# Kernel tuning notes

Hardware: AMD Instinct MI355X
Metric: run time of the kernel (lower is better)

Reference implementation:

```python
import jax, jax.numpy as jnp
import numpy as np

N_USERS = 50000
N_ENTITIES = 100000
N_NODES = N_USERS + N_ENTITIES
N_EDGES = 3000000
EMB_DIM = 64
WEIGHT_SIZES = [64, 64, 32, 16]  # [emb_dim] + weight_size
BATCH = 8192
LEAKY_SLOPE = 0.2  # KGAT (TF reference) uses leaky_relu alpha=0.2
EPS = 1e-12


def setup_inputs() -> dict:
    key = jax.random.key(0)
    ks = jax.random.split(key, 24)
    inp = {}
    inp["users"] = jax.random.randint(ks[0], (BATCH,), 0, N_USERS, dtype=jnp.int32)
    inp["pos_items"] = jax.random.randint(ks[1], (BATCH,), 0, N_ENTITIES, dtype=jnp.int32)
    inp["neg_items"] = jax.random.randint(ks[2], (BATCH,), 0, N_ENTITIES, dtype=jnp.int32)
    inp["all_h"] = jax.random.randint(ks[3], (N_EDGES,), 0, N_NODES, dtype=jnp.int32)
    inp["all_t"] = jax.random.randint(ks[4], (N_EDGES,), 0, N_NODES, dtype=jnp.int32)
    inp["A_values"] = jax.random.uniform(ks[5], (N_EDGES,), dtype=jnp.float32)
    inp["user_embed"] = jax.random.normal(ks[6], (N_USERS, EMB_DIM), dtype=jnp.float32) * 0.1
    inp["entity_embed"] = jax.random.normal(ks[7], (N_ENTITIES, EMB_DIM), dtype=jnp.float32) * 0.1
    ki = 8
    for k in range(3):
        din, dout = WEIGHT_SIZES[k], WEIGHT_SIZES[k + 1]
        scale = float(np.sqrt(2.0 / (din + dout)))  # xavier-ish
        inp[f"W_gc_{k}"] = jax.random.normal(ks[ki], (din, dout), dtype=jnp.float32) * scale; ki += 1
        inp[f"b_gc_{k}"] = jax.random.normal(ks[ki], (1, dout), dtype=jnp.float32) * scale; ki += 1
        inp[f"W_bi_{k}"] = jax.random.normal(ks[ki], (din, dout), dtype=jnp.float32) * scale; ki += 1
        inp[f"b_bi_{k}"] = jax.random.normal(ks[ki], (1, dout), dtype=jnp.float32) * scale; ki += 1
    return inp


def _bi_interaction(ego, all_h, all_t, A_values, layers, n_nodes):
    # KGAT bi-interaction aggregator over edge-list sparse adjacency.
    outs = [ego]
    for (W_gc, b_gc, W_bi, b_bi) in layers:
        # sparse A @ ego : gather tails, weight by attention, scatter-add to heads
        msgs = A_values[:, None] * ego[all_t]                       # [E, d]
        side = jax.ops.segment_sum(msgs, all_h, num_segments=n_nodes)  # [N, d]
        sum_emb = jax.nn.leaky_relu((ego + side) @ W_gc + b_gc, negative_slope=LEAKY_SLOPE)
        bi_emb = jax.nn.leaky_relu((ego * side) @ W_bi + b_bi, negative_slope=LEAKY_SLOPE)
        ego = sum_emb + bi_emb
        norm = ego / jnp.maximum(jnp.linalg.norm(ego, axis=1, keepdims=True), EPS)
        outs.append(norm)
    return jnp.concatenate(outs, axis=1)  # [N, 64+64+32+16]


def reference(users, pos_items, neg_items, all_h, all_t, A_values,
              user_embed, entity_embed,
              W_gc_0, b_gc_0, W_bi_0, b_bi_0,
              W_gc_1, b_gc_1, W_bi_1, b_bi_1,
              W_gc_2, b_gc_2, W_bi_2, b_bi_2):
    n_users = user_embed.shape[0]
    n_nodes = n_users + entity_embed.shape[0]
    ego = jnp.concatenate([user_embed, entity_embed], axis=0)  # [N, 64]
    layers = [(W_gc_0, b_gc_0, W_bi_0, b_bi_0),
              (W_gc_1, b_gc_1, W_bi_1, b_bi_1),
              (W_gc_2, b_gc_2, W_bi_2, b_bi_2)]
    all_emb = _bi_interaction(ego, all_h, all_t, A_values, layers, n_nodes)
    ua, ea = all_emb[:n_users], all_emb[n_users:]
    u_e = ua[users]
    pos_i_e = ea[pos_items]
    neg_i_e = ea[neg_items]
    return (u_e, pos_i_e, neg_i_e)
```

## Files before the change

kernel.cpp:

```cpp
#include <hip/hip_runtime.h>
#include <math.h>

#define N_USERS    50000
#define N_ENTITIES 100000
#define N_NODES    150000
#define N_EDGES    3000000
#define BATCH      8192
#define SLOPE      0.2f
#define EPSF       1e-12f

#define NBUK   2344
#define CAP    1536
#define STR    2560
#define PADM   16
#define BLK_E  12288
#define NPB    ((N_EDGES + BLK_E - 1) / BLK_E)
#define PBLK   1024
#define EPT    (BLK_E / PBLK)
#define CH     4096
#define PFW    (NBUK + 1)
#define CASTB  ((N_NODES * 64 / 4 + PBLK - 1) / PBLK)

__device__ __forceinline__ unsigned f2bf(float f) {
    unsigned u = __float_as_uint(f);
    return (u + 0x7FFFu + ((u >> 16) & 1u)) >> 16;
}
__device__ __forceinline__ float bf_lo(unsigned d) { return __uint_as_float(d << 16); }
__device__ __forceinline__ float bf_hi(unsigned d) { return __uint_as_float(d); }

__global__ __launch_bounds__(PBLK)
void prep_k(const int* __restrict__ all_h, const int* __restrict__ all_t,
            const float* __restrict__ A,
            int* __restrict__ prefix, int2* __restrict__ rec_src,
            const float* __restrict__ user_emb, const float* __restrict__ ent_emb,
            unsigned short* __restrict__ ego0_bf) {
    __shared__ int pos[NBUK];
    __shared__ int wsum[PBLK / 64];
    __shared__ int2 srec[CH];

    int t = threadIdx.x;

    if (blockIdx.x >= NPB) {
        int idx = (blockIdx.x - NPB) * PBLK + t;
        const int total = N_NODES * 64 / 4;
        if (idx >= total) return;
        int ge = idx * 4;
        const float* src = (ge < N_USERS * 64) ? user_emb + ge
                                               : ent_emb + (ge - N_USERS * 64);
        float4 v = *(const float4*)src;
        ushort4 o;
        o.x = (unsigned short)f2bf(v.x);
        o.y = (unsigned short)f2bf(v.y);
        o.z = (unsigned short)f2bf(v.z);
        o.w = (unsigned short)f2bf(v.w);
        *(ushort4*)(ego0_bf + ge) = o;
        return;
    }

    for (int i = t; i < NBUK; i += PBLK) pos[i] = 0;
    __syncthreads();

    int e0 = blockIdx.x * BLK_E;
    int e1 = e0 + BLK_E; if (e1 > N_EDGES) e1 = N_EDGES;
    int tot = e1 - e0;

    int h[EPT]; int tt[EPT]; float aa[EPT];
    #pragma unroll
    for (int k = 0; k < EPT; ++k) {
        int e = e0 + k * PBLK + t;
        bool v = e < e1;
        h[k]  = v ? all_h[e] : -1;
        tt[k] = v ? all_t[e] : 0;
        aa[k] = v ? A[e] : 0.f;
    }
    #pragma unroll
    for (int k = 0; k < EPT; ++k)
        if (h[k] >= 0) atomicAdd(&pos[h[k] >> 6], 1);
    __syncthreads();

    int c[3];
    int i0 = t * 3;
    int tsum = 0;
    #pragma unroll
    for (int j = 0; j < 3; ++j) {
        int idx = i0 + j;
        c[j] = (idx < NBUK) ? pos[idx] : 0;
        tsum += c[j];
    }

    int lane = t & 63, w = t >> 6;
    int incl = tsum;
    #pragma unroll
    for (int off = 1; off < 64; off <<= 1) {
        int x = __shfl_up(incl, off, 64);
        if (lane >= off) incl += x;
    }
    if (lane == 63) wsum[w] = incl;
    __syncthreads();
    int wbase = 0;
    for (int j = 0; j < w; ++j) wbase += wsum[j];
    int excl = wbase + (incl - tsum);

    size_t prow = (size_t)blockIdx.x * PFW;
    #pragma unroll
    for (int j = 0; j < 3; ++j) {
        int idx = i0 + j;
        if (idx < NBUK) { pos[idx] = excl; prefix[prow + idx] = excl; }
        excl += c[j];
    }
    if (t == PBLK - 1) prefix[prow + NBUK] = excl;
    __syncthreads();

    int pp[EPT];
    #pragma unroll
    for (int k = 0; k < EPT; ++k)
        pp[k] = (h[k] >= 0) ? atomicAdd(&pos[h[k] >> 6], 1) : -1;

    for (int base = 0; base < tot; base += CH) {
        __syncthreads();
        int lim = tot - base; if (lim > CH) lim = CH;
        #pragma unroll
        for (int k = 0; k < EPT; ++k) {
            int s = pp[k] - base;
            if (s >= 0 && s < CH)
                srec[s] = make_int2(tt[k] | ((h[k] & 63) << 18), __float_as_int(aa[k]));
        }
        __syncthreads();
        const int4* s4 = (const int4*)srec;
        int4* d4 = (int4*)(rec_src + e0 + base);
        int lim2 = lim >> 1;
        for (int s = t; s < lim2; s += PBLK) d4[s] = s4[s];
    }
}

__global__ __launch_bounds__(256)
void local_sort_k(const int* __restrict__ prefix, const int2* __restrict__ rec_src,
                  int2* __restrict__ rec, int2* __restrict__ range) {
    __shared__ int2 sin[CAP];
    __shared__ int2 sout[STR];
    __shared__ int cnt64[64];
    __shared__ int pos64[64];
    __shared__ int sc[256];
    __shared__ int s_ptot;
    int b = blockIdx.x, t = threadIdx.x;

    if (t < 64) cnt64[t] = 0;

    int rstart = 0, n_t = 0;
    if (t < NPB) {
        const int* prow = prefix + (size_t)t * PFW + b;
        int s0 = prow[0];
        int s1 = prow[1];
        rstart = t * BLK_E + s0;
        n_t = s1 - s0;
    }
    sc[t] = n_t;
    __syncthreads();

    for (int off = 1; off < 256; off <<= 1) {
        int v = sc[t];
        int u = (t >= off) ? sc[t - off] : 0;
        __syncthreads();
        sc[t] = v + u;
        __syncthreads();
    }
    int cnt = sc[255]; if (cnt > CAP) cnt = CAP;

    if (t < NPB && n_t > 0) {
        int d = sc[t] - n_t;
        for (int j = 0; j < n_t; ++j) {
            int dj = d + j;
            if (dj >= CAP) break;
            int2 p = rec_src[rstart + j];
            sin[dj] = p;
            atomicAdd(&cnt64[(p.x >> 18) & 63], 1);
        }
    }
    __syncthreads();

    if (t < 64) {
        int v = cnt64[t];
        int pv = (v + PADM - 1) & ~(PADM - 1);
        int sum = pv;
        #pragma unroll
        for (int off = 1; off < 64; off <<= 1) {
            int x = __shfl_up(sum, off, 64);
            if (t >= off) sum += x;
        }
        pos64[t] = sum - pv;
        if (t == 63) s_ptot = sum;
    }
    __syncthreads();
    int ptot = s_ptot;

    for (int i = t; i < ptot; i += 256) sout[i] = make_int2(0, 0);
    __syncthreads();

    for (int i = t; i < cnt; i += 256) {
        int2 p = sin[i];
        int l = (p.x >> 18) & 63;
        int dst = atomicAdd(&pos64[l], 1);
        sout[dst] = make_int2(p.x & 0x3FFFF, p.y);
    }
    __syncthreads();

    for (int i = t; i < ptot; i += 256)
        rec[(size_t)b * STR + i] = sout[i];

    if (t < 64) {
        int v = cnt64[t];
        int pv = (v + PADM - 1) & ~(PADM - 1);
        int sum = pv;
        #pragma unroll
        for (int off = 1; off < 64; off <<= 1) {
            int x = __shfl_up(sum, off, 64);
            if (t >= off) sum += x;
        }
        int start = b * STR + (sum - pv);
        int node = b * 64 + t;
        if (node < N_NODES) range[node] = make_int2(start, start + pv);
    }
}

template<int DIN>
__global__ __launch_bounds__(256)
void side_k(const int2* __restrict__ range, const int2* __restrict__ rec,
            const unsigned short* __restrict__ tab, float* __restrict__ side) {
    constexpr int LPR = DIN / 8;
    constexpr int EPW = 64 / LPR;

    int w = threadIdx.x >> 6;
    int lane = threadIdx.x & 63;
    int h = blockIdx.x * 4 + w;

    int2 rg = range[h];
    int e0 = rg.x, e1 = rg.y;
    int g = lane / LPR;
    int q = lane % LPR;

    float acc[8];
    #pragma unroll
    for (int j = 0; j < 8; ++j) acc[j] = 0.f;

    int e = e0;
    for (; e + 2 * EPW <= e1; e += 2 * EPW) {
        int2 p0 = rec[e + g];
        int2 p1 = rec[e + EPW + g];
        float a0 = __int_as_float(p0.y);
        float a1 = __int_as_float(p1.y);
        uint4 d0 = *(const uint4*)(tab + (unsigned)(p0.x * DIN) + q * 8);
        uint4 d1 = *(const uint4*)(tab + (unsigned)(p1.x * DIN) + q * 8);
        acc[0] = fmaf(a0, bf_lo(d0.x), acc[0]);
        acc[1] = fmaf(a0, bf_hi(d0.x), acc[1]);
        acc[2] = fmaf(a0, bf_lo(d0.y), acc[2]);
        acc[3] = fmaf(a0, bf_hi(d0.y), acc[3]);
        acc[4] = fmaf(a0, bf_lo(d0.z), acc[4]);
        acc[5] = fmaf(a0, bf_hi(d0.z), acc[5]);
        acc[6] = fmaf(a0, bf_lo(d0.w), acc[6]);
        acc[7] = fmaf(a0, bf_hi(d0.w), acc[7]);
        acc[0] = fmaf(a1, bf_lo(d1.x), acc[0]);
        acc[1] = fmaf(a1, bf_hi(d1.x), acc[1]);
        acc[2] = fmaf(a1, bf_lo(d1.y), acc[2]);
        acc[3] = fmaf(a1, bf_hi(d1.y), acc[3]);
        acc[4] = fmaf(a1, bf_lo(d1.z), acc[4]);
        acc[5] = fmaf(a1, bf_hi(d1.z), acc[5]);
        acc[6] = fmaf(a1, bf_lo(d1.w), acc[6]);
        acc[7] = fmaf(a1, bf_hi(d1.w), acc[7]);
    }
    if (e < e1) {
        int2 p0 = rec[e + g];
        float a0 = __int_as_float(p0.y);
        uint4 d0 = *(const uint4*)(tab + (unsigned)(p0.x * DIN) + q * 8);
        acc[0] = fmaf(a0, bf_lo(d0.x), acc[0]);
        acc[1] = fmaf(a0, bf_hi(d0.x), acc[1]);
        acc[2] = fmaf(a0, bf_lo(d0.y), acc[2]);
        acc[3] = fmaf(a0, bf_hi(d0.y), acc[3]);
        acc[4] = fmaf(a0, bf_lo(d0.z), acc[4]);
        acc[5] = fmaf(a0, bf_hi(d0.z), acc[5]);
        acc[6] = fmaf(a0, bf_lo(d0.w), acc[6]);
        acc[7] = fmaf(a0, bf_hi(d0.w), acc[7]);
    }

    #pragma unroll
    for (int off = LPR; off < 64; off <<= 1)
        #pragma unroll
        for (int j = 0; j < 8; ++j) acc[j] += __shfl_xor(acc[j], off, 64);

    if (lane < LPR) {
        float* dst = side + (size_t)h * DIN + q * 8;
        *(float4*)dst       = make_float4(acc[0], acc[1], acc[2], acc[3]);
        *(float4*)(dst + 4) = make_float4(acc[4], acc[5], acc[6], acc[7]);
    }
}

template<int DIN, int DOUT, int TILE_ROWS, bool CONCAT>
__global__ __launch_bounds__(256)
void transform_k(const unsigned short* __restrict__ ego_in,
                 const float* __restrict__ user_emb, const float* __restrict__ ent_emb,
                 const float* __restrict__ side,
                 const float* __restrict__ Wgc, const float* __restrict__ bgc,
                 const float* __restrict__ Wbi, const float* __restrict__ bbi,
                 unsigned short* __restrict__ ego_out) {
    constexpr int NG = DOUT / 8;
    constexpr int RG = 256 / NG;
    constexpr int RT = TILE_ROWS / RG;
    constexpr int STRIDE = DIN + 4;
    constexpr int KC8 = DIN / 8;

    __shared__ float sWgc[DIN * DOUT], sWbi[DIN * DOUT];
    __shared__ float sU[TILE_ROWS * STRIDE], sV[TILE_ROWS * STRIDE];

    int t = threadIdx.x;

    for (int i = t * 4; i < DIN * DOUT; i += 1024) {
        *(float4*)&sWgc[i] = *(const float4*)&Wgc[i];
        *(float4*)&sWbi[i] = *(const float4*)&Wbi[i];
    }

    int base = blockIdx.x * TILE_ROWS;
    for (int f = t; f < TILE_ROWS * KC8; f += 256) {
        int row = f / KC8, c8 = f % KC8;
        int n = base + row;
        int nc = n < N_NODES ? n : N_NODES - 1;
        float ev[8];
        if (CONCAT) {
            const float* erow = (nc < N_USERS) ? user_emb + (size_t)nc * 64
                                               : ent_emb + (size_t)(nc - N_USERS) * 64;
            float4 a = *(const float4*)(erow + c8 * 8);
            float4 b = *(const float4*)(erow + c8 * 8 + 4);
            ev[0] = a.x; ev[1] = a.y; ev[2] = a.z; ev[3] = a.w;
            ev[4] = b.x; ev[5] = b.y; ev[6] = b.z; ev[7] = b.w;
        } else {
            uint4 d = *(const uint4*)(ego_in + (size_t)nc * DIN + c8 * 8);
            ev[0] = bf_lo(d.x); ev[1] = bf_hi(d.x);
            ev[2] = bf_lo(d.y); ev[3] = bf_hi(d.y);
            ev[4] = bf_lo(d.z); ev[5] = bf_hi(d.z);
            ev[6] = bf_lo(d.w); ev[7] = bf_hi(d.w);
        }
        const float* srow = side + (size_t)nc * DIN + c8 * 8;
        float4 s0 = *(const float4*)srow;
        float4 s1 = *(const float4*)(srow + 4);
        float sv8[8] = {s0.x, s0.y, s0.z, s0.w, s1.x, s1.y, s1.z, s1.w};
        float* pu = &sU[row * STRIDE + c8 * 8];
        float* pv = &sV[row * STRIDE + c8 * 8];
        *(float4*)pu       = make_float4(ev[0] + sv8[0], ev[1] + sv8[1], ev[2] + sv8[2], ev[3] + sv8[3]);
        *(float4*)(pu + 4) = make_float4(ev[4] + sv8[4], ev[5] + sv8[5], ev[6] + sv8[6], ev[7] + sv8[7]);
        *(float4*)pv       = make_float4(ev[0] * sv8[0], ev[1] * sv8[1], ev[2] * sv8[2], ev[3] * sv8[3]);
        *(float4*)(pv + 4) = make_float4(ev[4] * sv8[4], ev[5] * sv8[5], ev[6] * sv8[6], ev[7] * sv8[7]);
    }
    __syncthreads();

    int cg = t % NG, rgi = t / NG;
    int c0 = cg * 8;
    int r0 = rgi * RT;

    float accg[RT][8], accb[RT][8];
    #pragma unroll
    for (int r = 0; r < RT; ++r)
        #pragma unroll
        for (int j = 0; j < 8; ++j) { accg[r][j] = 0.f; accb[r][j] = 0.f; }

    for (int k = 0; k < DIN; k += 4) {
        float4 u4[RT], v4[RT];
        #pragma unroll
        for (int r = 0; r < RT; ++r) {
            u4[r] = *(const float4*)&sU[(r0 + r) * STRIDE + k];
            v4[r] = *(const float4*)&sV[(r0 + r) * STRIDE + k];
        }
        #pragma unroll
        for (int kk = 0; kk < 4; ++kk) {
            float4 wg0 = *(const float4*)&sWgc[(k + kk) * DOUT + c0];
            float4 wg1 = *(const float4*)&sWgc[(k + kk) * DOUT + c0 + 4];
            float4 wb0 = *(const float4*)&sWbi[(k + kk) * DOUT + c0];
            float4 wb1 = *(const float4*)&sWbi[(k + kk) * DOUT + c0 + 4];
            #pragma unroll
            for (int r = 0; r < RT; ++r) {
                float u = ((const float*)&u4[r])[kk];
                float v = ((const float*)&v4[r])[kk];
                accg[r][0] = fmaf(u, wg0.x, accg[r][0]);
                accg[r][1] = fmaf(u, wg0.y, accg[r][1]);
                accg[r][2] = fmaf(u, wg0.z, accg[r][2]);
                accg[r][3] = fmaf(u, wg0.w, accg[r][3]);
                accg[r][4] = fmaf(u, wg1.x, accg[r][4]);
                accg[r][5] = fmaf(u, wg1.y, accg[r][5]);
                accg[r][6] = fmaf(u, wg1.z, accg[r][6]);
                accg[r][7] = fmaf(u, wg1.w, accg[r][7]);
                accb[r][0] = fmaf(v, wb0.x, accb[r][0]);
                accb[r][1] = fmaf(v, wb0.y, accb[r][1]);
                accb[r][2] = fmaf(v, wb0.z, accb[r][2]);
                accb[r][3] = fmaf(v, wb0.w, accb[r][3]);
                accb[r][4] = fmaf(v, wb1.x, accb[r][4]);
                accb[r][5] = fmaf(v, wb1.y, accb[r][5]);
                accb[r][6] = fmaf(v, wb1.z, accb[r][6]);
                accb[r][7] = fmaf(v, wb1.w, accb[r][7]);
            }
        }
    }

    float4 bg0 = *(const float4*)&bgc[c0];
    float4 bg1 = *(const float4*)&bgc[c0 + 4];
    float4 bb0 = *(const float4*)&bbi[c0];
    float4 bb1 = *(const float4*)&bbi[c0 + 4];
    float bg[8] = {bg0.x, bg0.y, bg0.z, bg0.w, bg1.x, bg1.y, bg1.z, bg1.w};
    float bb[8] = {bb0.x, bb0.y, bb0.z, bb0.w, bb1.x, bb1.y, bb1.z, bb1.w};

    #pragma unroll
    for (int r = 0; r < RT; ++r) {
        int n = base + r0 + r;
        if (n < N_NODES) {
            float o[8];
            #pragma unroll
            for (int j = 0; j < 8; ++j) {
                float gg = accg[r][j] + bg[j];
                float b2 = accb[r][j] + bb[j];
                gg = gg > 0.f ? gg : SLOPE * gg;
                b2 = b2 > 0.f ? b2 : SLOPE * b2;
                o[j] = gg + b2;
            }
            unsigned short* dst = ego_out + (size_t)n * DOUT + c0;
            uint4 wv;
            wv.x = f2bf(o[0]) | (f2bf(o[1]) << 16);
            wv.y = f2bf(o[2]) | (f2bf(o[3]) << 16);
            wv.z = f2bf(o[4]) | (f2bf(o[5]) << 16);
            wv.w = f2bf(o[6]) | (f2bf(o[7]) << 16);
            *(uint4*)dst = wv;
        }
    }
}

__global__ __launch_bounds__(256)
void final_k(const int* __restrict__ users, const int* __restrict__ pos,
             const int* __restrict__ neg,
             const float* __restrict__ user_emb, const float* __restrict__ ent_emb,
             const unsigned short* __restrict__ ego1_bf,
             const unsigned short* __restrict__ ego2_bf,
             const int2* __restrict__ range, const int2* __restrict__ rec,
             const float* __restrict__ Wgc, const float* __restrict__ bgc,
             const float* __restrict__ Wbi, const float* __restrict__ bbi,
             float* __restrict__ out) {
    __shared__ float sWgc[32 * 16], sWbi[32 * 16];
    int t = threadIdx.x;
    for (int i = t; i < 32 * 16; i += 256) { sWgc[i] = Wgc[i]; sWbi[i] = Wbi[i]; }
    __syncthreads();

    int w = t >> 6, lane = t & 63;
    int r = blockIdx.x * 4 + w;
    int which = r / BATCH;
    int i = r - which * BATCH;
    int node;
    if (which == 0)      node = users[i];
    else if (which == 1) node = N_USERS + pos[i];
    else                 node = N_USERS + neg[i];

    float* o = out + (size_t)r * 176;

    float x0 = (node < N_USERS) ? user_emb[(size_t)node * 64 + lane]
                                : ent_emb[(size_t)(node - N_USERS) * 64 + lane];
    o[lane] = x0;

    float x1 = __uint_as_float((unsigned)ego1_bf[(size_t)node * 64 + lane] << 16);
    float ss = x1 * x1;
    #pragma unroll
    for (int off = 32; off > 0; off >>= 1) ss += __shfl_xor(ss, off, 64);
    o[64 + lane] = x1 / fmaxf(sqrtf(ss), EPSF);

    float x2 = (lane < 32)
        ? __uint_as_float((unsigned)ego2_bf[(size_t)node * 32 + lane] << 16) : 0.f;
    float ss2 = x2 * x2;
    #pragma unroll
    for (int off = 32; off > 0; off >>= 1) ss2 += __shfl_xor(ss2, off, 64);
    if (lane < 32) o[128 + lane] = x2 / fmaxf(sqrtf(ss2), EPSF);

    constexpr int LPR = 4, EPW = 16;
    int g = lane / LPR, q = lane % LPR;
    int2 rg = range[node];
    int e0 = rg.x, e1 = rg.y;

    float acc[8];
    #pragma unroll
    for (int j = 0; j < 8; ++j) acc[j] = 0.f;

    int e = e0;
    for (; e + 2 * EPW <= e1; e += 2 * EPW) {
        int2 p0 = rec[e + g];
        int2 p1 = rec[e + EPW + g];
        float a0 = __int_as_float(p0.y);
        float a1 = __int_as_float(p1.y);
        uint4 d0 = *(const uint4*)(ego2_bf + (unsigned)(p0.x * 32) + q * 8);
        uint4 d1 = *(const uint4*)(ego2_bf + (unsigned)(p1.x * 32) + q * 8);
        acc[0] = fmaf(a0, bf_lo(d0.x), acc[0]);
        acc[1] = fmaf(a0, bf_hi(d0.x), acc[1]);
        acc[2] = fmaf(a0, bf_lo(d0.y), acc[2]);
        acc[3] = fmaf(a0, bf_hi(d0.y), acc[3]);
        acc[4] = fmaf(a0, bf_lo(d0.z), acc[4]);
        acc[5] = fmaf(a0, bf_hi(d0.z), acc[5]);
        acc[6] = fmaf(a0, bf_lo(d0.w), acc[6]);
        acc[7] = fmaf(a0, bf_hi(d0.w), acc[7]);
        acc[0] = fmaf(a1, bf_lo(d1.x), acc[0]);
        acc[1] = fmaf(a1, bf_hi(d1.x), acc[1]);
        acc[2] = fmaf(a1, bf_lo(d1.y), acc[2]);
        acc[3] = fmaf(a1, bf_hi(d1.y), acc[3]);
        acc[4] = fmaf(a1, bf_lo(d1.z), acc[4]);
        acc[5] = fmaf(a1, bf_hi(d1.z), acc[5]);
        acc[6] = fmaf(a1, bf_lo(d1.w), acc[6]);
        acc[7] = fmaf(a1, bf_hi(d1.w), acc[7]);
    }
    if (e < e1) {
        int2 p0 = rec[e + g];
        float a0 = __int_as_float(p0.y);
        uint4 d0 = *(const uint4*)(ego2_bf + (unsigned)(p0.x * 32) + q * 8);
        acc[0] = fmaf(a0, bf_lo(d0.x), acc[0]);
        acc[1] = fmaf(a0, bf_hi(d0.x), acc[1]);
        acc[2] = fmaf(a0, bf_lo(d0.y), acc[2]);
        acc[3] = fmaf(a0, bf_hi(d0.y), acc[3]);
        acc[4] = fmaf(a0, bf_lo(d0.z), acc[4]);
        acc[5] = fmaf(a0, bf_hi(d0.z), acc[5]);
        acc[6] = fmaf(a0, bf_lo(d0.w), acc[6]);
        acc[7] = fmaf(a0, bf_hi(d0.w), acc[7]);
    }

    #pragma unroll
    for (int off = LPR; off < 64; off <<= 1)
        #pragma unroll
        for (int j = 0; j < 8; ++j) acc[j] += __shfl_xor(acc[j], off, 64);

    uint4 dd = *(const uint4*)(ego2_bf + (size_t)node * 32 + q * 8);
    float Uc[8], Vc[8];
    {
        float ev[8] = { bf_lo(dd.x), bf_hi(dd.x), bf_lo(dd.y), bf_hi(dd.y),
                        bf_lo(dd.z), bf_hi(dd.z), bf_lo(dd.w), bf_hi(dd.w) };
        #pragma unroll
        for (int j = 0; j < 8; ++j) { Uc[j] = ev[j] + acc[j]; Vc[j] = ev[j] * acc[j]; }
    }

    if (lane < 16) {
        float accg = 0.f, accb = 0.f;
        #pragma unroll
        for (int k = 0; k < 32; ++k) {
            float u = __shfl(Uc[k & 7], k >> 3, 64);
            float v = __shfl(Vc[k & 7], k >> 3, 64);
            accg = fmaf(u, sWgc[k * 16 + lane], accg);
            accb = fmaf(v, sWbi[k * 16 + lane], accb);
        }
        float gg = accg + bgc[lane];
        float b2 = accb + bbi[lane];
        gg = gg > 0.f ? gg : SLOPE * gg;
        b2 = b2 > 0.f ? b2 : SLOPE * b2;
        float x3 = gg + b2;
        float ss3 = x3 * x3;
        #pragma unroll
        for (int off = 8; off > 0; off >>= 1) ss3 += __shfl_xor(ss3, off, 64);
        o[160 + lane] = x3 / fmaxf(sqrtf(ss3), EPSF);
    }
}

extern "C" void kernel_launch(void* const* d_in, const int* in_sizes, int n_in,
                              void* d_out, int out_size, void* d_ws, size_t ws_size,
                              hipStream_t stream) {
    const int*   users    = (const int*)d_in[0];
    const int*   pos      = (const int*)d_in[1];
    const int*   neg      = (const int*)d_in[2];
    const int*   all_h    = (const int*)d_in[3];
    const int*   all_t    = (const int*)d_in[4];
    const float* A        = (const float*)d_in[5];
    const float* user_emb = (const float*)d_in[6];
    const float* ent_emb  = (const float*)d_in[7];
    const float* Wgc0 = (const float*)d_in[8];
    const float* bgc0 = (const float*)d_in[9];
    const float* Wbi0 = (const float*)d_in[10];
    const float* bbi0 = (const float*)d_in[11];
    const float* Wgc1 = (const float*)d_in[12];
    const float* bgc1 = (const float*)d_in[13];
    const float* Wbi1 = (const float*)d_in[14];
    const float* bbi1 = (const float*)d_in[15];
    const float* Wgc2 = (const float*)d_in[16];
    const float* bgc2 = (const float*)d_in[17];
    const float* Wbi2 = (const float*)d_in[18];
    const float* bbi2 = (const float*)d_in[19];

    char* p = (char*)d_ws;
    int*   prefix  = (int*)p;            p += ((size_t)NPB * PFW * 4 + 255) & ~255ull;
    float* side    = (float*)p;
    int2*  rec_src = (int2*)p;           p += ((size_t)N_NODES * 64 * 4 + 255) & ~255ull;
    int2*  rec     = (int2*)p;           p += ((size_t)NBUK * STR * 8 + 255) & ~255ull;
    int2*  range   = (int2*)p;           p += ((size_t)N_NODES * 8 + 255) & ~255ull;
    unsigned short* ego0_bf = (unsigned short*)p; p += ((size_t)N_NODES * 64 * 2 + 255) & ~255ull;
    unsigned short* ego1_bf = (unsigned short*)p; p += ((size_t)N_NODES * 64 * 2 + 255) & ~255ull;
    unsigned short* ego2_bf = (unsigned short*)p; p += ((size_t)N_NODES * 32 * 2 + 255) & ~255ull;
    float* out     = (float*)d_out;

    const int nodeBlocks = N_NODES / 4;

    prep_k<<<NPB + CASTB, PBLK, 0, stream>>>(all_h, all_t, A, prefix, rec_src,
                                             user_emb, ent_emb, ego0_bf);
    local_sort_k<<<NBUK, 256, 0, stream>>>(prefix, rec_src, rec, range);

    side_k<64><<<nodeBlocks, 256, 0, stream>>>(range, rec, ego0_bf, side);
    transform_k<64, 64, 64, true><<<(N_NODES + 63) / 64, 256, 0, stream>>>(
        nullptr, user_emb, ent_emb, side, Wgc0, bgc0, Wbi0, bbi0, ego1_bf);

    side_k<64><<<nodeBlocks, 256, 0, stream>>>(range, rec, ego1_bf, side);
    transform_k<64, 32, 64, false><<<(N_NODES + 63) / 64, 256, 0, stream>>>(
        ego1_bf, nullptr, nullptr, side, Wgc1, bgc1, Wbi1, bbi1, ego2_bf);

    final_k<<<3 * BATCH / 4, 256, 0, stream>>>(
        users, pos, neg, user_emb, ent_emb, ego1_bf, ego2_bf,
        range, rec, Wgc2, bgc2, Wbi2, bbi2, out);
}
```

Baseline: 442.0 us.

## Fuse sparse aggregation with per-node dense transform into one layer kernel

Merges side_k and transform_k so each wavefront aggregates neighbor messages for one node, then applies both weight matrices via shuffles and LDS-resident weights. This removes the fp32 side buffer write/read round trip and one launch per layer. The per-node matvec uses 64 shuffle steps per wave with low reuse of the weights, and the odd-edge tail handling is dropped on the assumption that ranges are padded to multiples of 16. Each block also reloads full weights for only 4 nodes.

Measured after the change: 832.7 us. 1.88x slower.

```diff
diff --git a/kernel.cpp b/kernel.cpp
--- a/kernel.cpp
+++ b/kernel.cpp
@@ -222,21 +222,31 @@
     }
 }
 
-template<int DIN>
+template<int DOUT, bool CONCAT>
 __global__ __launch_bounds__(256)
-void side_k(const int2* __restrict__ range, const int2* __restrict__ rec,
-            const unsigned short* __restrict__ tab, float* __restrict__ side) {
-    constexpr int LPR = DIN / 8;
-    constexpr int EPW = 64 / LPR;
-
-    int w = threadIdx.x >> 6;
-    int lane = threadIdx.x & 63;
-    int h = blockIdx.x * 4 + w;
-
-    int2 rg = range[h];
+void fused_layer_k(const int2* __restrict__ range, const int2* __restrict__ rec,
+                   const unsigned short* __restrict__ tab,
+                   const float* __restrict__ user_emb, const float* __restrict__ ent_emb,
+                   const float* __restrict__ Wgc, const float* __restrict__ bgc,
+                   const float* __restrict__ Wbi, const float* __restrict__ bbi,
+                   unsigned short* __restrict__ ego_out) {
+    constexpr int DIN = 64;
+    constexpr int LPR = 8, EPW = 8;
+
+    __shared__ float sWgc[DIN * DOUT], sWbi[DIN * DOUT];
+    int t = threadIdx.x;
+    for (int i = t * 4; i < DIN * DOUT; i += 1024) {
+        *(float4*)&sWgc[i] = *(const float4*)&Wgc[i];
+        *(float4*)&sWbi[i] = *(const float4*)&Wbi[i];
+    }
+    __syncthreads();
+
+    int w = t >> 6, lane = t & 63;
+    int node = blockIdx.x * 4 + w;
+    int g = lane / LPR, q = lane % LPR;
+
+    int2 rg = range[node];
     int e0 = rg.x, e1 = rg.y;
-    int g = lane / LPR;
-    int q = lane % LPR;
 
     float acc[8];
     #pragma unroll
@@ -267,164 +277,65 @@
         acc[6] = fmaf(a1, bf_lo(d1.w), acc[6]);
         acc[7] = fmaf(a1, bf_hi(d1.w), acc[7]);
     }
-    if (e < e1) {
-        int2 p0 = rec[e + g];
-        float a0 = __int_as_float(p0.y);
-        uint4 d0 = *(const uint4*)(tab + (unsigned)(p0.x * DIN) + q * 8);
-        acc[0] = fmaf(a0, bf_lo(d0.x), acc[0]);
-        acc[1] = fmaf(a0, bf_hi(d0.x), acc[1]);
-        acc[2] = fmaf(a0, bf_lo(d0.y), acc[2]);
-        acc[3] = fmaf(a0, bf_hi(d0.y), acc[3]);
-        acc[4] = fmaf(a0, bf_lo(d0.z), acc[4]);
-        acc[5] = fmaf(a0, bf_hi(d0.z), acc[5]);
-        acc[6] = fmaf(a0, bf_lo(d0.w), acc[6]);
-        acc[7] = fmaf(a0, bf_hi(d0.w), acc[7]);
-    }
 
     #pragma unroll
     for (int off = LPR; off < 64; off <<= 1)
         #pragma unroll
         for (int j = 0; j < 8; ++j) acc[j] += __shfl_xor(acc[j], off, 64);
 
-    if (lane < LPR) {
-        float* dst = side + (size_t)h * DIN + q * 8;
-        *(float4*)dst       = make_float4(acc[0], acc[1], acc[2], acc[3]);
-        *(float4*)(dst + 4) = make_float4(acc[4], acc[5], acc[6], acc[7]);
-    }
-}
-
-template<int DIN, int DOUT, int TILE_ROWS, bool CONCAT>
-__global__ __launch_bounds__(256)
-void transform_k(const unsigned short* __restrict__ ego_in,
-                 const float* __restrict__ user_emb, const float* __restrict__ ent_emb,
-                 const float* __restrict__ side,
-                 const float* __restrict__ Wgc, const float* __restrict__ bgc,
-                 const float* __restrict__ Wbi, const float* __restrict__ bbi,
-                 unsigned short* __restrict__ ego_out) {
-    constexpr int NG = DOUT / 8;
-    constexpr int RG = 256 / NG;
-    constexpr int RT = TILE_ROWS / RG;
-    constexpr int STRIDE = DIN + 4;
-    constexpr int KC8 = DIN / 8;
-
-    __shared__ float sWgc[DIN * DOUT], sWbi[DIN * DOUT];
-    __shared__ float sU[TILE_ROWS * STRIDE], sV[TILE_ROWS * STRIDE];
-
-    int t = threadIdx.x;
-
-    for (int i = t * 4; i < DIN * DOUT; i += 1024) {
-        *(float4*)&sWgc[i] = *(const float4*)&Wgc[i];
-        *(float4*)&sWbi[i] = *(const float4*)&Wbi[i];
-    }
-
-    int base = blockIdx.x * TILE_ROWS;
-    for (int f = t; f < TILE_ROWS * KC8; f += 256) {
-        int row = f / KC8, c8 = f % KC8;
-        int n = base + row;
-        int nc = n < N_NODES ? n : N_NODES - 1;
+    float Uc[8], Vc[8];
+    {
         float ev[8];
         if (CONCAT) {
-            const float* erow = (nc < N_USERS) ? user_emb + (size_t)nc * 64
-                                               : ent_emb + (size_t)(nc - N_USERS) * 64;
-            float4 a = *(const float4*)(erow + c8 * 8);
-            float4 b = *(const float4*)(erow + c8 * 8 + 4);
+            const float* erow = (node < N_USERS)
+                ? user_emb + (size_t)node * 64
+                : ent_emb + (size_t)(node - N_USERS) * 64;
+            float4 a = *(const float4*)(erow + q * 8);
+            float4 b = *(const float4*)(erow + q * 8 + 4);
             ev[0] = a.x; ev[1] = a.y; ev[2] = a.z; ev[3] = a.w;
             ev[4] = b.x; ev[5] = b.y; ev[6] = b.z; ev[7] = b.w;
         } else {
-            uint4 d = *(const uint4*)(ego_in + (size_t)nc * DIN + c8 * 8);
+            uint4 d = *(const uint4*)(tab + (unsigned)(node * DIN) + q * 8);
             ev[0] = bf_lo(d.x); ev[1] = bf_hi(d.x);
             ev[2] = bf_lo(d.y); ev[3] = bf_hi(d.y);
             ev[4] = bf_lo(d.z); ev[5] = bf_hi(d.z);
             ev[6] = bf_lo(d.w); ev[7] = bf_hi(d.w);
         }
-        const float* srow = side + (size_t)nc * DIN + c8 * 8;
-        float4 s0 = *(const float4*)srow;
-        float4 s1 = *(const float4*)(srow + 4);
-        float sv8[8] = {s0.x, s0.y, s0.z, s0.w, s1.x, s1.y, s1.z, s1.w};
-        float* pu = &sU[row * STRIDE + c8 * 8];
-        float* pv = &sV[row * STRIDE + c8 * 8];
-        *(float4*)pu       = make_float4(ev[0] + sv8[0], ev[1] + sv8[1], ev[2] + sv8[2], ev[3] + sv8[3]);
-        *(float4*)(pu + 4) = make_float4(ev[4] + sv8[4], ev[5] + sv8[5], ev[6] + sv8[6], ev[7] + sv8[7]);
-        *(float4*)pv       = make_float4(ev[0] * sv8[0], ev[1] * sv8[1], ev[2] * sv8[2], ev[3] * sv8[3]);
-        *(float4*)(pv + 4) = make_float4(ev[4] * sv8[4], ev[5] * sv8[5], ev[6] * sv8[6], ev[7] * sv8[7]);
-    }
-    __syncthreads();
-
-    int cg = t % NG, rgi = t / NG;
-    int c0 = cg * 8;
-    int r0 = rgi * RT;
-
-    float accg[RT][8], accb[RT][8];
-    #pragma unroll
-    for (int r = 0; r < RT; ++r)
-        #pragma unroll
-        for (int j = 0; j < 8; ++j) { accg[r][j] = 0.f; accb[r][j] = 0.f; }
-
-    for (int k = 0; k < DIN; k += 4) {
-        float4 u4[RT], v4[RT];
-        #pragma unroll
-        for (int r = 0; r < RT; ++r) {
-            u4[r] = *(const float4*)&sU[(r0 + r) * STRIDE + k];
-            v4[r] = *(const float4*)&sV[(r0 + r) * STRIDE + k];
-        }
-        #pragma unroll
-        for (int kk = 0; kk < 4; ++kk) {
-            float4 wg0 = *(const float4*)&sWgc[(k + kk) * DOUT + c0];
-            float4 wg1 = *(const float4*)&sWgc[(k + kk) * DOUT + c0 + 4];
-            float4 wb0 = *(const float4*)&sWbi[(k + kk) * DOUT + c0];
-            float4 wb1 = *(const float4*)&sWbi[(k + kk) * DOUT + c0 + 4];
-            #pragma unroll
-            for (int r = 0; r < RT; ++r) {
-                float u = ((const float*)&u4[r])[kk];
-                float v = ((const float*)&v4[r])[kk];
-                accg[r][0] = fmaf(u, wg0.x, accg[r][0]);
-                accg[r][1] = fmaf(u, wg0.y, accg[r][1]);
-                accg[r][2] = fmaf(u, wg0.z, accg[r][2]);
-                accg[r][3] = fmaf(u, wg0.w, accg[r][3]);
-                accg[r][4] = fmaf(u, wg1.x, accg[r][4]);
-                accg[r][5] = fmaf(u, wg1.y, accg[r][5]);
-                accg[r][6] = fmaf(u, wg1.z, accg[r][6]);
-                accg[r][7] = fmaf(u, wg1.w, accg[r][7]);
-                accb[r][0] = fmaf(v, wb0.x, accb[r][0]);
-                accb[r][1] = fmaf(v, wb0.y, accb[r][1]);
-                accb[r][2] = fmaf(v, wb0.z, accb[r][2]);
-                accb[r][3] = fmaf(v, wb0.w, accb[r][3]);
-                accb[r][4] = fmaf(v, wb1.x, accb[r][4]);
-                accb[r][5] = fmaf(v, wb1.y, accb[r][5]);
-                accb[r][6] = fmaf(v, wb1.z, accb[r][6]);
-                accb[r][7] = fmaf(v, wb1.w, accb[r][7]);
-            }
-        }
-    }
-
-    float4 bg0 = *(const float4*)&bgc[c0];
-    float4 bg1 = *(const float4*)&bgc[c0 + 4];
-    float4 bb0 = *(const float4*)&bbi[c0];
-    float4 bb1 = *(const float4*)&bbi[c0 + 4];
-    float bg[8] = {bg0.x, bg0.y, bg0.z, bg0.w, bg1.x, bg1.y, bg1.z, bg1.w};
-    float bb[8] = {bb0.x, bb0.y, bb0.z, bb0.w, bb1.x, bb1.y, bb1.z, bb1.w};
-
-    #pragma unroll
-    for (int r = 0; r < RT; ++r) {
-        int n = base + r0 + r;
-        if (n < N_NODES) {
-            float o[8];
-            #pragma unroll
-            for (int j = 0; j < 8; ++j) {
-                float gg = accg[r][j] + bg[j];
-                float b2 = accb[r][j] + bb[j];
-                gg = gg > 0.f ? gg : SLOPE * gg;
-                b2 = b2 > 0.f ? b2 : SLOPE * b2;
-                o[j] = gg + b2;
-            }
-            unsigned short* dst = ego_out + (size_t)n * DOUT + c0;
-            uint4 wv;
-            wv.x = f2bf(o[0]) | (f2bf(o[1]) << 16);
-            wv.y = f2bf(o[2]) | (f2bf(o[3]) << 16);
-            wv.z = f2bf(o[4]) | (f2bf(o[5]) << 16);
-            wv.w = f2bf(o[6]) | (f2bf(o[7]) << 16);
-            *(uint4*)dst = wv;
-        }
+        #pragma unroll
+        for (int j = 0; j < 8; ++j) { Uc[j] = ev[j] + acc[j]; Vc[j] = ev[j] * acc[j]; }
+    }
+
+    if (DOUT == 64) {
+        float accg = 0.f, accb = 0.f;
+        #pragma unroll
+        for (int k = 0; k < 64; ++k) {
+            float u = __shfl(Uc[k & 7], k >> 3, 64);
+            float v = __shfl(Vc[k & 7], k >> 3, 64);
+            accg = fmaf(u, sWgc[k * 64 + lane], accg);
+            accb = fmaf(v, sWbi[k * 64 + lane], accb);
+        }
+        float gg = accg + bgc[lane];
+        float b2 = accb + bbi[lane];
+        gg = gg > 0.f ? gg : SLOPE * gg;
+        b2 = b2 > 0.f ? b2 : SLOPE * b2;
+        ego_out[(size_t)node * 64 + lane] = (unsigned short)f2bf(gg + b2);
+    } else {
+        int c = lane & 31, half = lane >> 5;
+        float acc2 = 0.f;
+        #pragma unroll
+        for (int k = 0; k < 64; ++k) {
+            float u = __shfl(Uc[k & 7], k >> 3, 64);
+            float v = __shfl(Vc[k & 7], k >> 3, 64);
+            float x = half ? v : u;
+            const float* W = half ? sWbi : sWgc;
+            acc2 = fmaf(x, W[k * 32 + c], acc2);
+        }
+        float bias = half ? bbi[c] : bgc[c];
+        float t2 = acc2 + bias;
+        t2 = t2 > 0.f ? t2 : SLOPE * t2;
+        float other = __shfl(t2, lane ^ 32, 64);
+        if (half == 0)
+            ego_out[(size_t)node * 32 + c] = (unsigned short)f2bf(t2 + other);
     }
 }
 
@@ -580,8 +491,7 @@
 
     char* p = (char*)d_ws;
     int*   prefix  = (int*)p;            p += ((size_t)NPB * PFW * 4 + 255) & ~255ull;
-    float* side    = (float*)p;
-    int2*  rec_src = (int2*)p;           p += ((size_t)N_NODES * 64 * 4 + 255) & ~255ull;
+    int2*  rec_src = (int2*)p;           p += ((size_t)N_EDGES * 8 + 255) & ~255ull;
     int2*  rec     = (int2*)p;           p += ((size_t)NBUK * STR * 8 + 255) & ~255ull;
     int2*  range   = (int2*)p;           p += ((size_t)N_NODES * 8 + 255) & ~255ull;
     unsigned short* ego0_bf = (unsigned short*)p; p += ((size_t)N_NODES * 64 * 2 + 255) & ~255ull;
@@ -595,13 +505,11 @@
                                              user_emb, ent_emb, ego0_bf);
     local_sort_k<<<NBUK, 256, 0, stream>>>(prefix, rec_src, rec, range);
 
-    side_k<64><<<nodeBlocks, 256, 0, stream>>>(range, rec, ego0_bf, side);
-    transform_k<64, 64, 64, true><<<(N_NODES + 63) / 64, 256, 0, stream>>>(
-        nullptr, user_emb, ent_emb, side, Wgc0, bgc0, Wbi0, bbi0, ego1_bf);
-
-    side_k<64><<<nodeBlocks, 256, 0, stream>>>(range, rec, ego1_bf, side);
-    transform_k<64, 32, 64, false><<<(N_NODES + 63) / 64, 256, 0, stream>>>(
-        ego1_bf, nullptr, nullptr, side, Wgc1, bgc1, Wbi1, bbi1, ego2_bf);
+    fused_layer_k<64, true><<<nodeBlocks, 256, 0, stream>>>(
+        range, rec, ego0_bf, user_emb, ent_emb, Wgc0, bgc0, Wbi0, bbi0, ego1_bf);
+
+    fused_layer_k<32, false><<<nodeBlocks, 256, 0, stream>>>(
+        range, rec, ego1_bf, nullptr, nullptr, Wgc1, bgc1, Wbi1, bbi1, ego2_bf);
 
     final_k<<<3 * BATCH / 4, 256, 0, stream>>>(
         users, pos, neg, user_emb, ent_emb, ego1_bf, ego2_bf,
```
